# Performance work log

Hardware: AMD Instinct MI355X
Metric: run time of the kernel (lower is better)

## Reference

```python
import jax, jax.numpy as jnp
import numpy as np

NUM_HEADS = 8
NUM_GROUPS = 32
EPS = 1e-5


def setup_inputs() -> dict:
    key = jax.random.key(0)
    k1, k2, k3 = jax.random.split(key, 3)
    B, C, H, W = 2, 512, 64, 64
    x = jax.random.normal(k1, (B, C, H, W), dtype=jnp.float32)
    gn_weight = jnp.ones((C,), dtype=jnp.float32)
    gn_bias = jnp.zeros((C,), dtype=jnp.float32)
    # small init so softmax logits are well-conditioned
    w_qkv = jax.random.normal(k2, (3 * C, C), dtype=jnp.float32) * 0.02
    w_proj = jax.random.normal(k3, (C, C), dtype=jnp.float32) * 0.02
    b_proj = jnp.zeros((C,), dtype=jnp.float32)
    return {"x": x, "gn_weight": gn_weight, "gn_bias": gn_bias,
            "w_qkv": w_qkv, "w_proj": w_proj, "b_proj": b_proj}


def group_norm(x, weight, bias):
    B, C, H, W = x.shape
    xg = x.reshape(B, NUM_GROUPS, C // NUM_GROUPS, H, W)
    mean = xg.mean(axis=(2, 3, 4), keepdims=True)
    var = xg.var(axis=(2, 3, 4), keepdims=True)
    xg = (xg - mean) * jax.lax.rsqrt(var + EPS)
    x = xg.reshape(B, C, H, W)
    return x * weight[None, :, None, None] + bias[None, :, None, None]


def reference(x, gn_weight, gn_bias, w_qkv, w_proj, b_proj):
    B, C, H, W = x.shape
    nh = NUM_HEADS
    hd = C // nh
    N = H * W

    h = group_norm(x, gn_weight, gn_bias)
    # 1x1 conv == per-pixel matmul: [B,3C,H,W]
    qkv = jnp.einsum('bchw,oc->bohw', h, w_qkv)
    # (B,3,nh,hd,N) -> (3,B,nh,N,hd)
    qkv = qkv.reshape(B, 3, nh, hd, N).transpose(1, 0, 2, 4, 3)
    q, k, v = qkv[0], qkv[1], qkv[2]

    scale = hd ** -0.5
    attn = jax.nn.softmax(jnp.einsum('bhnd,bhmd->bhnm', q, k) * scale, axis=-1)
    out = jnp.einsum('bhnm,bhmd->bhnd', attn, v)  # [B,nh,N,hd]
    out = out.transpose(0, 1, 3, 2).reshape(B, C, H, W)
    out = jnp.einsum('bchw,oc->bohw', out, w_proj) + b_proj[None, :, None, None]
    return x + out
```

## Files before the change

kernel.cpp:

```cpp
#include <hip/hip_runtime.h>
#include <math.h>

#define BB 2
#define CC 512
#define NN 4096
#define NH 8
#define HD 64
#define NG 32
#define CPG 16

typedef __attribute__((ext_vector_type(8))) short short8;
typedef __attribute__((ext_vector_type(4))) float f32x4;
typedef __attribute__((ext_vector_type(16))) float f32x16;
typedef __attribute__((ext_vector_type(2))) unsigned int u32x2;

typedef __attribute__((address_space(1))) void glb_t;
typedef __attribute__((address_space(3))) void lds_t;

__device__ __forceinline__ void async16(const void* g, void* l) {
  __builtin_amdgcn_global_load_lds((const glb_t*)g, (lds_t*)l, 16, 0, 0);
}

__device__ __forceinline__ unsigned short f2bf(float f) {
  unsigned int u = __float_as_uint(f);
  u += 0x7fffu + ((u >> 16) & 1u);
  return (unsigned short)(u >> 16);
}

__device__ __forceinline__ unsigned int cvt_pk_bf16(float a, float b) {
  unsigned int r;
  asm("v_cvt_pk_bf16_f32 %0, %1, %2" : "=v"(r) : "v"(a), "v"(b));
  return r;
}

__global__ __launch_bounds__(256) void k_gnstats(const float* __restrict__ x,
                                                 float* __restrict__ stats) {
  int b = blockIdx.x >> 5, g = blockIdx.x & 31;
  const float4* p = (const float4*)(x + (size_t)(b * CC + g * CPG) * NN);
  double s = 0.0, sq = 0.0;
  for (int i = threadIdx.x; i < (CPG * NN) / 4; i += 256) {
    float4 v = p[i];
    s  += (double)v.x + (double)v.y + (double)v.z + (double)v.w;
    sq += (double)v.x * v.x + (double)v.y * v.y + (double)v.z * v.z + (double)v.w * v.w;
  }
  __shared__ double red[512];
  red[threadIdx.x] = s; red[256 + threadIdx.x] = sq;
  __syncthreads();
  for (int off = 128; off > 0; off >>= 1) {
    if (threadIdx.x < off) {
      red[threadIdx.x] += red[threadIdx.x + off];
      red[256 + threadIdx.x] += red[256 + threadIdx.x + off];
    }
    __syncthreads();
  }
  if (threadIdx.x == 0) {
    double mean = red[0] / (double)(CPG * NN);
    double var  = red[256] / (double)(CPG * NN) - mean * mean;
    stats[(b * NG + g) * 2]     = (float)mean;
    stats[(b * NG + g) * 2 + 1] = (float)(1.0 / sqrt(var + 1e-5));
  }
}

__global__ __launch_bounds__(256) void k_gnapply(const float* __restrict__ x,
                                                 const float* __restrict__ gw,
                                                 const float* __restrict__ gb,
                                                 const float* __restrict__ stats,
                                                 unsigned short* __restrict__ hT) {
  int bid = blockIdx.x;
  int b = bid >> 9;
  int c0 = ((bid >> 6) & 7) * 64;
  int n0 = (bid & 63) * 64;
  __shared__ float tile[64 * 65];
  int t = threadIdx.x;
#pragma unroll
  for (int i = 0; i < 16; ++i) {
    int e = i * 256 + t, c = e >> 6, n = e & 63;
    int cg = c0 + c, g = cg >> 4;
    float mu = stats[(b * NG + g) * 2], rs = stats[(b * NG + g) * 2 + 1];
    float v = x[(size_t)(b * CC + cg) * NN + n0 + n];
    tile[c * 65 + n] = (v - mu) * rs * gw[cg] + gb[cg];
  }
  __syncthreads();
#pragma unroll
  for (int i = 0; i < 16; ++i) {
    int e = i * 256 + t, n = e >> 6, c = e & 63;
    hT[(size_t)(b * NN + n0 + n) * CC + c0 + c] = f2bf(tile[c * 65 + n]);
  }
}

__global__ __launch_bounds__(256) void k_cvt(const float* __restrict__ src,
                                             unsigned short* __restrict__ dst) {
  int i = (blockIdx.x * 256 + threadIdx.x) * 4;
  float4 v = *(const float4*)(src + i);
  ushort4 o;
  o.x = f2bf(v.x); o.y = f2bf(v.y); o.z = f2bf(v.z); o.w = f2bf(v.w);
  *(ushort4*)(dst + i) = o;
}

__device__ __forceinline__ void gemm_mainloop(const unsigned short* __restrict__ A,
                                              const unsigned short* __restrict__ Bm,
                                              char* smem, int m0, int n0,
                                              f32x4 acc[4][4]) {
  const int t = threadIdx.x, wave = t >> 6, lane = t & 63;
  const int l15 = lane & 15, lhi = lane >> 4;
  const int wr = wave >> 1, wc = wave & 1;
  const f32x4 fz = {0.f, 0.f, 0.f, 0.f};
#pragma unroll
  for (int mi = 0; mi < 4; ++mi)
#pragma unroll
    for (int ni = 0; ni < 4; ++ni) acc[mi][ni] = fz;

  for (int kt = 0; kt < 8; ++kt) {
    __syncthreads();
#pragma unroll
    for (int issue = 0; issue < 4; ++issue) {
      int slot = issue * 256 + t;
      int row = slot >> 3, g = slot & 7;
      async16(A + (size_t)(m0 + row) * 512 + kt * 64 + g * 8,
              smem + issue * 4096 + wave * 1024);
      async16(Bm + (size_t)(n0 + row) * 512 + kt * 64 + g * 8,
              smem + 16384 + issue * 4096 + wave * 1024);
    }
    __syncthreads();
#pragma unroll
    for (int kk = 0; kk < 2; ++kk) {
      short8 a[4], bf[4];
#pragma unroll
      for (int mi = 0; mi < 4; ++mi)
        a[mi] = *(const short8*)(smem + (wr * 64 + mi * 16 + l15) * 128 + kk * 64 + lhi * 16);
#pragma unroll
      for (int ni = 0; ni < 4; ++ni)
        bf[ni] = *(const short8*)(smem + 16384 + (wc * 64 + ni * 16 + l15) * 128 + kk * 64 + lhi * 16);
#pragma unroll
      for (int mi = 0; mi < 4; ++mi)
#pragma unroll
        for (int ni = 0; ni < 4; ++ni)
          acc[mi][ni] = __builtin_amdgcn_mfma_f32_16x16x32_bf16(a[mi], bf[ni], acc[mi][ni], 0, 0, 0);
    }
  }
}

__global__ __launch_bounds__(256) void k_qkvgemm(const unsigned short* __restrict__ hT,
                                                 const unsigned short* __restrict__ Wq,
                                                 unsigned short* __restrict__ qkv) {
  __shared__ char smem[32768];
  f32x4 acc[4][4];
  int m0 = blockIdx.x * 128, n0 = blockIdx.y * 128;
  gemm_mainloop(hT, Wq, smem, m0, n0, acc);
  const int t = threadIdx.x, wave = t >> 6, lane = t & 63;
  const int l15 = lane & 15, lhi = lane >> 4;
  const int wr = wave >> 1, wc = wave & 1;
#pragma unroll
  for (int mi = 0; mi < 4; ++mi)
#pragma unroll
    for (int ni = 0; ni < 4; ++ni)
#pragma unroll
      for (int r = 0; r < 4; ++r) {
        int m = m0 + wr * 64 + mi * 16 + lhi * 4 + r;
        int o = n0 + wc * 64 + ni * 16 + l15;
        qkv[(size_t)m * 1536 + o] = f2bf(acc[mi][ni][r]);
      }
}

__global__ __launch_bounds__(256) void k_vtrans(const unsigned short* __restrict__ qkv,
                                                unsigned short* __restrict__ vT) {
  int bid = blockIdx.x;
  int bh = bid >> 6, n0 = (bid & 63) * 64;
  int b = bh >> 3, h = bh & 7;
  __shared__ unsigned short tile[64 * 65];
  int t = threadIdx.x;
#pragma unroll
  for (int i = 0; i < 16; ++i) {
    int e = i * 256 + t, n = e >> 6, d = e & 63;
    tile[d * 65 + n] = qkv[(size_t)(b * NN + n0 + n) * 1536 + 1024 + h * 64 + d];
  }
  __syncthreads();
#pragma unroll
  for (int i = 0; i < 16; ++i) {
    int e = i * 256 + t, d = e >> 6, n = e & 63;
    vT[(size_t)(bh * 64 + d) * NN + n0 + n] = tile[d * 65 + n];
  }
}

__global__ __launch_bounds__(128) void k_attn(const unsigned short* __restrict__ qkv,
                                              const unsigned short* __restrict__ vT,
                                              unsigned short* __restrict__ att) {
  __shared__ char smem[32768];
  const int t = threadIdx.x, wave = t >> 6, lane = t & 63;
  const int l31 = lane & 31, lh = lane >> 5;
  int bid0 = blockIdx.x;
  int bid = (bid0 & 7) * 128 + (bid0 >> 3);
  int bh = bid >> 6, q0 = (bid & 63) * 64;
  int b = bh >> 3, h = bh & 7;
  const float C = 0.125f * 1.4426950408889634f;

#pragma unroll
  for (int i = 0; i < 4; ++i) {
    int slot = i * 128 + t, row = slot >> 3, g = slot & 7;
    int gs = (g ^ (row & 7)) * 8;
    async16(qkv + (size_t)(b * NN + q0 + row) * 1536 + h * 64 + gs,
            smem + 16384 + i * 2048 + wave * 1024);
    async16(qkv + (size_t)(b * NN + row) * 1536 + 512 + h * 64 + gs,
            smem + i * 2048 + wave * 1024);
    async16(vT + (size_t)(bh * 64 + row) * NN + gs,
            smem + 8192 + i * 2048 + wave * 1024);
  }

  int koff[2][4];
#pragma unroll
  for (int tt = 0; tt < 2; ++tt)
#pragma unroll
    for (int kk = 0; kk < 4; ++kk)
      koff[tt][kk] = tt * 4096 + l31 * 128 + ((((kk << 1) + lh) ^ (l31 & 7)) << 4);

  int rowb = t >> 3, g0 = t & 7;
  int gsb = (g0 ^ (rowb & 7)) * 8;
  const char* kSrc = (const char*)(qkv + (size_t)(b * NN + 64 + rowb) * 1536 + 512 + h * 64 + gsb);
  const char* vSrc = (const char*)(vT + (size_t)(bh * 64 + rowb) * NN + 64 + gsb);

  __syncthreads();
  short8 qa[4];
#pragma unroll
  for (int kk = 0; kk < 4; ++kk)
    qa[kk] = *(const short8*)(smem + 16384 + wave * 4096 + (koff[0][kk] & 4095));
  __syncthreads();

  f32x16 o[2];
  o[0] = (f32x16)0.f; o[1] = (f32x16)0.f;
  float lsum = 0.f;

#define ATTN_BODY(CURB, NXTB)                                                          \
  {                                                                                    \
    _Pragma("unroll")                                                                  \
    for (int i = 0; i < 4; ++i) {                                                      \
      async16(kSrc + i * 49152,  smem + (NXTB) + i * 2048 + wave * 1024);              \
      async16(vSrc + i * 131072, smem + (NXTB) + 8192 + i * 2048 + wave * 1024);       \
    }                                                                                  \
    kSrc += 196608; vSrc += 128;                                                       \
    f32x16 sT[2];                                                                      \
    __builtin_amdgcn_s_setprio(1);                                                     \
    _Pragma("unroll")                                                                  \
    for (int tt = 0; tt < 2; ++tt) {                                                   \
      sT[tt] = (f32x16)0.f;                                                            \
      _Pragma("unroll")                                                                \
      for (int kk = 0; kk < 4; ++kk) {                                                 \
        short8 ka = *(const short8*)(smem + (CURB) + koff[tt][kk]);                    \
        sT[tt] = __builtin_amdgcn_mfma_f32_32x32x16_bf16(ka, qa[kk], sT[tt], 0, 0, 0); \
      }                                                                                \
    }                                                                                  \
    __builtin_amdgcn_s_setprio(0);                                                     \
    float ls0 = 0.f, ls1 = 0.f;                                                        \
    _Pragma("unroll")                                                                  \
    for (int tt = 0; tt < 2; ++tt)                                                     \
      _Pragma("unroll")                                                                \
      for (int r = 0; r < 16; r += 2) {                                                \
        sT[tt][r]     = __builtin_amdgcn_exp2f(sT[tt][r] * C);                         \
        sT[tt][r + 1] = __builtin_amdgcn_exp2f(sT[tt][r + 1] * C);                     \
        ls0 += sT[tt][r]; ls1 += sT[tt][r + 1];                                        \
      }                                                                                \
    lsum += ls0 + ls1;                                                                 \
    __builtin_amdgcn_s_setprio(1);                                                     \
    _Pragma("unroll")                                                                  \
    for (int kk = 0; kk < 4; ++kk) {                                                   \
      int tt = kk >> 1, rb = (kk & 1) * 8;                                             \
      unsigned int x0 = cvt_pk_bf16(sT[tt][rb],     sT[tt][rb + 1]);                   \
      unsigned int x1 = cvt_pk_bf16(sT[tt][rb + 2], sT[tt][rb + 3]);                   \
      unsigned int x2 = cvt_pk_bf16(sT[tt][rb + 4], sT[tt][rb + 5]);                   \
      unsigned int x3 = cvt_pk_bf16(sT[tt][rb + 6], sT[tt][rb + 7]);                   \
      unsigned int u0 = x0, u1 = x1, u2 = x2, u3 = x3;                                 \
      asm("v_permlane32_swap_b32 %0, %1" : "+v"(x0), "+v"(u0));                        \
      asm("v_permlane32_swap_b32 %0, %1" : "+v"(x1), "+v"(u1));                        \
      asm("v_permlane32_swap_b32 %0, %1" : "+v"(x2), "+v"(u2));                        \
      asm("v_permlane32_swap_b32 %0, %1" : "+v"(x3), "+v"(u3));                        \
      union { unsigned int d[4]; short8 s; } pb;                                       \
      pb.d[0] = lh ? x2 : x0;                                                          \
      pb.d[1] = lh ? x3 : x1;                                                          \
      pb.d[2] = lh ? u2 : u0;                                                          \
      pb.d[3] = lh ? u3 : u1;                                                          \
      _Pragma("unroll")                                                                \
      for (int dt = 0; dt < 2; ++dt) {                                                 \
        short8 va = *(const short8*)(smem + (CURB) + 8192 + koff[dt][kk]);             \
        o[dt] = __builtin_amdgcn_mfma_f32_32x32x16_bf16(va, pb.s, o[dt], 0, 0, 0);     \
      }                                                                                \
    }                                                                                  \
    __builtin_amdgcn_s_setprio(0);                                                     \
    __syncthreads();                                                                   \
  }

  for (int it2 = 0; it2 < 32; ++it2) {
    ATTN_BODY(0, 16384)
    ATTN_BODY(16384, 0)
  }
#undef ATTN_BODY

  lsum += __shfl_xor(lsum, 32, 64);
  float rl = 1.f / lsum;
  unsigned short* abase = att + (size_t)(b * NN + q0 + wave * 32 + l31) * CC + h * 64 + 4 * lh;
#pragma unroll
  for (int dt = 0; dt < 2; ++dt)
#pragma unroll
    for (int rp = 0; rp < 8; ++rp) {
      unsigned int w = cvt_pk_bf16(o[dt][2 * rp] * rl, o[dt][2 * rp + 1] * rl);
      *(unsigned int*)(abase + 32 * dt + 8 * (rp >> 1) + 2 * (rp & 1)) = w;
    }
}

__global__ __launch_bounds__(256) void k_projgemm(const unsigned short* __restrict__ att,
                                                  const unsigned short* __restrict__ Wp,
                                                  const float* __restrict__ x,
                                                  const float* __restrict__ bproj,
                                                  float* __restrict__ out) {
  __shared__ char smem[33280];
  f32x4 acc[4][4];
  int m0 = blockIdx.x * 128, n0 = blockIdx.y * 128;
  gemm_mainloop(att, Wp, smem, m0, n0, acc);
  const int t = threadIdx.x, wave = t >> 6, lane = t & 63;
  const int l15 = lane & 15, lhi = lane >> 4;
  const int wr = wave >> 1, wc = wave & 1;
  __syncthreads();
  float* stg = (float*)(smem + wave * 8320);
  int b = m0 >> 12;
  int nbase = (m0 & 4095) + wr * 64;
#pragma unroll
  for (int half = 0; half < 2; ++half) {
#pragma unroll
    for (int nl = 0; nl < 2; ++nl) {
      int ni = half * 2 + nl;
#pragma unroll
      for (int mi = 0; mi < 4; ++mi)
#pragma unroll
        for (int r = 0; r < 4; ++r) {
          int cl = nl * 16 + l15;
          int row = mi * 16 + lhi * 4 + r;
          stg[cl * 65 + row] = acc[mi][ni][r];
        }
    }
#pragma unroll 4
    for (int i = 0; i < 32; ++i) {
      int oc = n0 + wc * 64 + half * 32 + i;
      float v = stg[i * 65 + lane];
      size_t idx = (size_t)(b * CC + oc) * NN + nbase + lane;
      out[idx] = x[idx] + v + bproj[oc];
    }
    __syncthreads();
  }
}

extern "C" void kernel_launch(void* const* d_in, const int* in_sizes, int n_in,
                              void* d_out, int out_size, void* d_ws, size_t ws_size,
                              hipStream_t stream) {
  const float* x     = (const float*)d_in[0];
  const float* gw    = (const float*)d_in[1];
  const float* gb    = (const float*)d_in[2];
  const float* wqkv  = (const float*)d_in[3];
  const float* wproj = (const float*)d_in[4];
  const float* bproj = (const float*)d_in[5];
  float* out = (float*)d_out;
  char* ws = (char*)d_ws;

  unsigned short* qkvb  = (unsigned short*)(ws + 0);
  unsigned short* vTb   = (unsigned short*)(ws + 25165824);
  unsigned short* attb  = (unsigned short*)(ws + 33554432);
  unsigned short* hTb   = (unsigned short*)(ws + 41943040);
  unsigned short* wqkvb = (unsigned short*)(ws + 50331648);
  unsigned short* wprojb= (unsigned short*)(ws + 51904512);
  float*          stats = (float*)(ws + 52428800);

  k_gnstats<<<64, 256, 0, stream>>>(x, stats);
  k_gnapply<<<1024, 256, 0, stream>>>(x, gw, gb, stats, hTb);
  k_cvt<<<768, 256, 0, stream>>>(wqkv, wqkvb);
  k_cvt<<<256, 256, 0, stream>>>(wproj, wprojb);
  k_qkvgemm<<<dim3(64, 12), 256, 0, stream>>>(hTb, wqkvb, qkvb);
  k_vtrans<<<1024, 256, 0, stream>>>(qkvb, vTb);
  k_attn<<<1024, 128, 0, stream>>>(qkvb, vTb, attb);
  k_projgemm<<<dim3(64, 4), 256, 0, stream>>>(attb, wprojb, x, bproj, out);
}
```

Baseline: 245.8 us.

## Split attention key tiles across wave pairs with LDS reduction of partial outputs

The attention kernel moves from 2 to 4 waves per block. Each pair of waves shares a 32-row query slice and splits every 64-key tile into two 32-key halves, so each wave does half the QK and PV MFMAs per iteration. At the end, one wave of each pair writes its partial output accumulators and row sum to LDS and the other adds them before normalising and storing. The LDS layout also changes from an XOR swizzle to a plain per-lane layout, which may bring bank conflicts. The change adds more waves per block for latency hiding, at the cost of an extra cross-wave reduction and more registers in flight per CU.

```diff
diff --git a/kernel.cpp b/kernel.cpp
--- a/kernel.cpp
+++ b/kernel.cpp
@@ -182,91 +182,83 @@
   }
 }
 
-__global__ __launch_bounds__(128) void k_attn(const unsigned short* __restrict__ qkv,
+__global__ __launch_bounds__(256) void k_attn(const unsigned short* __restrict__ qkv,
                                               const unsigned short* __restrict__ vT,
                                               unsigned short* __restrict__ att) {
   __shared__ char smem[32768];
   const int t = threadIdx.x, wave = t >> 6, lane = t & 63;
   const int l31 = lane & 31, lh = lane >> 5;
+  const int wq = wave >> 1, wk = wave & 1;
   int bid0 = blockIdx.x;
   int bid = (bid0 & 7) * 128 + (bid0 >> 3);
   int bh = bid >> 6, q0 = (bid & 63) * 64;
   int b = bh >> 3, h = bh & 7;
   const float C = 0.125f * 1.4426950408889634f;
 
-#pragma unroll
-  for (int i = 0; i < 4; ++i) {
-    int slot = i * 128 + t, row = slot >> 3, g = slot & 7;
-    int gs = (g ^ (row & 7)) * 8;
-    async16(qkv + (size_t)(b * NN + q0 + row) * 1536 + h * 64 + gs,
-            smem + 16384 + i * 2048 + wave * 1024);
-    async16(qkv + (size_t)(b * NN + row) * 1536 + 512 + h * 64 + gs,
-            smem + i * 2048 + wave * 1024);
-    async16(vT + (size_t)(bh * 64 + row) * NN + gs,
-            smem + 8192 + i * 2048 + wave * 1024);
-  }
-
-  int koff[2][4];
-#pragma unroll
-  for (int tt = 0; tt < 2; ++tt)
-#pragma unroll
-    for (int kk = 0; kk < 4; ++kk)
-      koff[tt][kk] = tt * 4096 + l31 * 128 + ((((kk << 1) + lh) ^ (l31 & 7)) << 4);
-
-  int rowb = t >> 3, g0 = t & 7;
-  int gsb = (g0 ^ (rowb & 7)) * 8;
-  const char* kSrc = (const char*)(qkv + (size_t)(b * NN + 64 + rowb) * 1536 + 512 + h * 64 + gsb);
-  const char* vSrc = (const char*)(vT + (size_t)(bh * 64 + rowb) * NN + 64 + gsb);
+  const unsigned short* kS[2];
+  const unsigned short* vS[2];
+#pragma unroll
+  for (int i = 0; i < 2; ++i) {
+    kS[i] = qkv + (size_t)(b * NN + i * 32 + l31) * 1536 + 512 + h * 64 + (wave * 2 + lh) * 8;
+    vS[i] = vT + (size_t)(bh * 64 + (wave & 1) * 32 + l31) * NN + ((i * 2 + (wave >> 1)) * 2 + lh) * 8;
+  }
+
+#pragma unroll
+  for (int i = 0; i < 2; ++i) {
+    async16(qkv + (size_t)(b * NN + q0 + i * 32 + l31) * 1536 + h * 64 + (wave * 2 + lh) * 8,
+            smem + 16384 + (i * 4 + wave) * 1024);
+    async16(kS[i], smem + (i * 4 + wave) * 1024);
+    async16(vS[i], smem + 8192 + (i * 4 + wave) * 1024);
+    kS[i] += 98304;
+    vS[i] += 64;
+  }
+
+  const int rbK = wk * 4096 + lh * 512 + l31 * 16;
+  const int rbV = 8192 + wk * 4096 + lh * 512 + l31 * 16;
+  const int rbQ = 16384 + wq * 4096 + lh * 512 + l31 * 16;
 
   __syncthreads();
   short8 qa[4];
 #pragma unroll
   for (int kk = 0; kk < 4; ++kk)
-    qa[kk] = *(const short8*)(smem + 16384 + wave * 4096 + (koff[0][kk] & 4095));
-  __syncthreads();
-
-  f32x16 o[2];
-  o[0] = (f32x16)0.f; o[1] = (f32x16)0.f;
+    qa[kk] = *(const short8*)(smem + rbQ + kk * 1024);
+  __syncthreads();
+
+  f32x16 o0 = (f32x16)0.f, o1 = (f32x16)0.f;
   float lsum = 0.f;
 
 #define ATTN_BODY(CURB, NXTB)                                                          \
   {                                                                                    \
     _Pragma("unroll")                                                                  \
-    for (int i = 0; i < 4; ++i) {                                                      \
-      async16(kSrc + i * 49152,  smem + (NXTB) + i * 2048 + wave * 1024);              \
-      async16(vSrc + i * 131072, smem + (NXTB) + 8192 + i * 2048 + wave * 1024);       \
+    for (int i = 0; i < 2; ++i) {                                                      \
+      async16(kS[i], smem + (NXTB) + (i * 4 + wave) * 1024);                           \
+      async16(vS[i], smem + (NXTB) + 8192 + (i * 4 + wave) * 1024);                    \
+      kS[i] += 98304; vS[i] += 64;                                                     \
     }                                                                                  \
-    kSrc += 196608; vSrc += 128;                                                       \
-    f32x16 sT[2];                                                                      \
+    f32x16 sT = (f32x16)0.f;                                                           \
     __builtin_amdgcn_s_setprio(1);                                                     \
     _Pragma("unroll")                                                                  \
-    for (int tt = 0; tt < 2; ++tt) {                                                   \
-      sT[tt] = (f32x16)0.f;                                                            \
-      _Pragma("unroll")                                                                \
-      for (int kk = 0; kk < 4; ++kk) {                                                 \
-        short8 ka = *(const short8*)(smem + (CURB) + koff[tt][kk]);                    \
-        sT[tt] = __builtin_amdgcn_mfma_f32_32x32x16_bf16(ka, qa[kk], sT[tt], 0, 0, 0); \
-      }                                                                                \
+    for (int kk = 0; kk < 4; ++kk) {                                                   \
+      short8 ka = *(const short8*)(smem + (CURB) + rbK + kk * 1024);                   \
+      sT = __builtin_amdgcn_mfma_f32_32x32x16_bf16(ka, qa[kk], sT, 0, 0, 0);           \
     }                                                                                  \
     __builtin_amdgcn_s_setprio(0);                                                     \
     float ls0 = 0.f, ls1 = 0.f;                                                        \
     _Pragma("unroll")                                                                  \
-    for (int tt = 0; tt < 2; ++tt)                                                     \
-      _Pragma("unroll")                                                                \
-      for (int r = 0; r < 16; r += 2) {                                                \
-        sT[tt][r]     = __builtin_amdgcn_exp2f(sT[tt][r] * C);                         \
-        sT[tt][r + 1] = __builtin_amdgcn_exp2f(sT[tt][r + 1] * C);                     \
-        ls0 += sT[tt][r]; ls1 += sT[tt][r + 1];                                        \
-      }                                                                                \
+    for (int r = 0; r < 16; r += 2) {                                                  \
+      sT[r]     = __builtin_amdgcn_exp2f(sT[r] * C);                                   \
+      sT[r + 1] = __builtin_amdgcn_exp2f(sT[r + 1] * C);                               \
+      ls0 += sT[r]; ls1 += sT[r + 1];                                                  \
+    }                                                                                  \
     lsum += ls0 + ls1;                                                                 \
     __builtin_amdgcn_s_setprio(1);                                                     \
     _Pragma("unroll")                                                                  \
-    for (int kk = 0; kk < 4; ++kk) {                                                   \
-      int tt = kk >> 1, rb = (kk & 1) * 8;                                             \
-      unsigned int x0 = cvt_pk_bf16(sT[tt][rb],     sT[tt][rb + 1]);                   \
-      unsigned int x1 = cvt_pk_bf16(sT[tt][rb + 2], sT[tt][rb + 3]);                   \
-      unsigned int x2 = cvt_pk_bf16(sT[tt][rb + 4], sT[tt][rb + 5]);                   \
-      unsigned int x3 = cvt_pk_bf16(sT[tt][rb + 6], sT[tt][rb + 7]);                   \
+    for (int kc = 0; kc < 2; ++kc) {                                                   \
+      int rb = kc * 8;                                                                 \
+      unsigned int x0 = cvt_pk_bf16(sT[rb],     sT[rb + 1]);                           \
+      unsigned int x1 = cvt_pk_bf16(sT[rb + 2], sT[rb + 3]);                           \
+      unsigned int x2 = cvt_pk_bf16(sT[rb + 4], sT[rb + 5]);                           \
+      unsigned int x3 = cvt_pk_bf16(sT[rb + 6], sT[rb + 7]);                           \
       unsigned int u0 = x0, u1 = x1, u2 = x2, u3 = x3;                                 \
       asm("v_permlane32_swap_b32 %0, %1" : "+v"(x0), "+v"(u0));                        \
       asm("v_permlane32_swap_b32 %0, %1" : "+v"(x1), "+v"(u1));                        \
@@ -277,11 +269,10 @@
       pb.d[1] = lh ? x3 : x1;                                                          \
       pb.d[2] = lh ? u2 : u0;                                                          \
       pb.d[3] = lh ? u3 : u1;                                                          \
-      _Pragma("unroll")                                                                \
-      for (int dt = 0; dt < 2; ++dt) {                                                 \
-        short8 va = *(const short8*)(smem + (CURB) + 8192 + koff[dt][kk]);             \
-        o[dt] = __builtin_amdgcn_mfma_f32_32x32x16_bf16(va, pb.s, o[dt], 0, 0, 0);     \
-      }                                                                                \
+      short8 va0 = *(const short8*)(smem + (CURB) + rbV + kc * 2048);                  \
+      o0 = __builtin_amdgcn_mfma_f32_32x32x16_bf16(va0, pb.s, o0, 0, 0, 0);            \
+      short8 va1 = *(const short8*)(smem + (CURB) + rbV + kc * 2048 + 1024);           \
+      o1 = __builtin_amdgcn_mfma_f32_32x32x16_bf16(va1, pb.s, o1, 0, 0, 0);            \
     }                                                                                  \
     __builtin_amdgcn_s_setprio(0);                                                     \
     __syncthreads();                                                                   \
@@ -294,15 +285,47 @@
 #undef ATTN_BODY
 
   lsum += __shfl_xor(lsum, 32, 64);
-  float rl = 1.f / lsum;
-  unsigned short* abase = att + (size_t)(b * NN + q0 + wave * 32 + l31) * CC + h * 64 + 4 * lh;
-#pragma unroll
-  for (int dt = 0; dt < 2; ++dt)
-#pragma unroll
-    for (int rp = 0; rp < 8; ++rp) {
-      unsigned int w = cvt_pk_bf16(o[dt][2 * rp] * rl, o[dt][2 * rp + 1] * rl);
-      *(unsigned int*)(abase + 32 * dt + 8 * (rp >> 1) + 2 * (rp & 1)) = w;
-    }
+  if (wk) {
+    char* os = smem + wq * 8192;
+#pragma unroll
+    for (int dt = 0; dt < 2; ++dt)
+#pragma unroll
+      for (int rp = 0; rp < 4; ++rp) {
+        f32x4 v;
+        v[0] = (dt ? o1 : o0)[4 * rp];     v[1] = (dt ? o1 : o0)[4 * rp + 1];
+        v[2] = (dt ? o1 : o0)[4 * rp + 2]; v[3] = (dt ? o1 : o0)[4 * rp + 3];
+        *(f32x4*)(os + (dt * 4 + rp) * 1024 + lane * 16) = v;
+      }
+    *(float*)(smem + 16384 + wq * 256 + lane * 4) = lsum;
+  }
+  __syncthreads();
+  if (!wk) {
+    float lt = lsum + *(const float*)(smem + 16384 + wq * 256 + lane * 4);
+    float rl = 1.f / lt;
+    const char* os = smem + wq * 8192;
+#pragma unroll
+    for (int dt = 0; dt < 2; ++dt)
+#pragma unroll
+      for (int rp = 0; rp < 4; ++rp) {
+        f32x4 v = *(const f32x4*)(os + (dt * 4 + rp) * 1024 + lane * 16);
+        if (dt) {
+          o1[4 * rp] += v[0]; o1[4 * rp + 1] += v[1];
+          o1[4 * rp + 2] += v[2]; o1[4 * rp + 3] += v[3];
+        } else {
+          o0[4 * rp] += v[0]; o0[4 * rp + 1] += v[1];
+          o0[4 * rp + 2] += v[2]; o0[4 * rp + 3] += v[3];
+        }
+      }
+    unsigned short* abase = att + (size_t)(b * NN + q0 + wq * 32 + l31) * CC + h * 64 + 4 * lh;
+#pragma unroll
+    for (int dt = 0; dt < 2; ++dt)
+#pragma unroll
+      for (int rp = 0; rp < 8; ++rp) {
+        float e0 = (dt ? o1 : o0)[2 * rp], e1 = (dt ? o1 : o0)[2 * rp + 1];
+        unsigned int w = cvt_pk_bf16(e0 * rl, e1 * rl);
+        *(unsigned int*)(abase + 32 * dt + 8 * (rp >> 1) + 2 * (rp & 1)) = w;
+      }
+  }
 }
 
 __global__ __launch_bounds__(256) void k_projgemm(const unsigned short* __restrict__ att,
@@ -372,6 +395,6 @@
   k_cvt<<<256, 256, 0, stream>>>(wproj, wprojb);
   k_qkvgemm<<<dim3(64, 12), 256, 0, stream>>>(hTb, wqkvb, qkvb);
   k_vtrans<<<1024, 256, 0, stream>>>(qkvb, vTb);
-  k_attn<<<1024, 128, 0, stream>>>(qkvb, vTb, attb);
+  k_attn<<<1024, 256, 0, stream>>>(qkvb, vTb, attb);
   k_projgemm<<<dim3(64, 4), 256, 0, stream>>>(attb, wprojb, x, bproj, out);
 }
```

Measured after the change: 298.9 us. +21.6%, slower.
